# Performance work log

Hardware: AMD Instinct MI355X
Metric: run time of the kernel (lower is better)

Reference implementation:

```python
import jax, jax.numpy as jnp
import numpy as np

B, C, H, W = 4, 16, 512, 512


def setup_inputs() -> dict:
    key = jax.random.key(0)
    k1, k2, k3, k4, k5 = jax.random.split(key, 5)
    # positive depth in [0.5, 10.5] meters
    depth = jax.random.uniform(k1, (B, 1, H, W), dtype=jnp.float32) * 10.0 + 0.5
    # realistic, well-conditioned camera intrinsics per batch element
    fx = 500.0 + 20.0 * jax.random.normal(k2, (B,), dtype=jnp.float32)
    fy = 500.0 + 20.0 * jax.random.normal(k3, (B,), dtype=jnp.float32)
    zeros = jnp.zeros((B,), jnp.float32)
    ones = jnp.ones((B,), jnp.float32)
    K = jnp.stack([
        jnp.stack([fx, zeros, ones * (W / 2.0)], axis=-1),
        jnp.stack([zeros, fy, ones * (H / 2.0)], axis=-1),
        jnp.stack([zeros, zeros, ones], axis=-1),
    ], axis=1)  # [B,3,3]
    # near-identity rigid-ish transforms so homogeneous w ~ 1
    T = jnp.eye(4, dtype=jnp.float32)[None, None] + 0.05 * jax.random.normal(k4, (B, C, 4, 4), dtype=jnp.float32)
    masks = jax.random.randint(k5, (B, C, H, W), 0, 2).astype(jnp.bool_)
    return {"depth": depth, "K": K, "T": T, "masks": masks}


def reference(depth, K, T, masks):
    b, _, h, w = depth.shape
    c = masks.shape[1]
    n = h * w
    eps = 1e-10
    # --- depth -> point cloud ---
    u = jnp.arange(w, dtype=depth.dtype)
    v = jnp.arange(h, dtype=depth.dtype)
    uu, vv = jnp.meshgrid(u, v, indexing='xy')            # [H,W]
    uv1 = jnp.stack([uu, vv, jnp.ones_like(uu)], axis=-1)  # [H,W,3]
    K_inv = jnp.linalg.inv(K)                              # [B,3,3]
    d = jnp.transpose(depth, (0, 2, 3, 1))                 # [B,H,W,1]
    points_3d = jnp.einsum('bij,hwj->bhwi', K_inv, uv1) * d  # [B,H,W,3]
    # --- per-object masked transform (vectorized over all channels) ---
    pts = points_3d.reshape(b, n, 3)
    pts_h = jnp.concatenate([pts, jnp.ones((b, n, 1), pts.dtype)], axis=-1)  # [B,N,4]
    trans_h = jnp.einsum('bcij,bnj->bcni', T, pts_h)       # [B,C,N,4]
    trans3 = trans_h[..., :3] / (trans_h[..., 3:] + eps)   # [B,C,N,3]
    masks_flat = masks.reshape(b, c, n)
    out = pts
    for ci in range(c):
        out = jnp.where(masks_flat[:, ci, :, None], trans3[:, ci], out)
    tp = out.reshape(b, h, w, 3)                           # transformed points
    # --- reproject to depth map (scatter) ---
    p2h = jnp.einsum('bij,bhwj->bhwi', K, tp)              # [B,H,W,3]
    p2 = p2h[..., :2] / (p2h[..., 2:] + eps)
    Z = tp[..., 2]                                         # [B,H,W]
    u_idx = jnp.clip(p2[..., 0], 0, w - 1).astype(jnp.int32)
    v_idx = jnp.clip(p2[..., 1], 0, h - 1).astype(jnp.int32)
    b_idx = jnp.broadcast_to(jnp.arange(b)[:, None, None], (b, h, w))
    depth_map = depth.at[b_idx, 0, v_idx, u_idx].set(Z)
    return depth_map
```

## Files before the change

kernel.cpp:

```cpp
#include <hip/hip_runtime.h>
#include <stdint.h>

constexpr int B = 4, C = 16, H = 512, W = 512;
constexpr int N = H * W;
constexpr int BLOCKS_PER_BATCH = N / 256;
constexpr int NXCD = 8;
constexpr float EPS = 1e-10f;


__device__ __forceinline__ void swizzle_bn(int orig, int& b, int& blk) {
    int xcd = orig & (NXCD - 1);
    int j   = orig >> 3;
    b       = j >> 7;
    int r   = j & 127;
    blk     = xcd * 128 + r;
}

constexpr int MSTRIDE = 260;

__global__ __launch_bounds__(256) void project_atomic_kernel(
    const float* __restrict__ depth,
    const float* __restrict__ K,
    const float* __restrict__ T,
    const int*   __restrict__ masks,
    unsigned long long* __restrict__ keys)
{
    __shared__ float Ts[16][17];
    __shared__ int   Ms[16 * MSTRIDE];

    int b, blk;
    swizzle_bn(blockIdx.x, b, blk);
    int t = threadIdx.x;
    int n = (blk << 8) + t;
    int idx = b * N + n;
    int v = n >> 9;
    int u = n & (W - 1);
    int lane = t & 63;

    {
        int w = t >> 6;
        int g = t & 63;
        const int* mbase = masks + (size_t)b * C * N + (size_t)(blk << 8);
        #pragma unroll
        for (int k = 0; k < 4; ++k) {
            int c = (w << 2) + k;
            int4 m4 = *reinterpret_cast<const int4*>(mbase + (size_t)c * N + (g << 2));
            *reinterpret_cast<int4*>(&Ms[c * MSTRIDE + (g << 2)]) = m4;
        }
    }

    float d = depth[idx];

    {
        int c = t >> 4, e = t & 15;
        Ts[e][c] = T[(size_t)b * 256 + t];
    }
    __syncthreads();

    unsigned bm = 0;
    #pragma unroll
    for (int c = 0; c < 16; ++c)
        bm |= (Ms[c * MSTRIDE + t] ? 1u : 0u) << c;
    int sel = bm ? (31 - __clz(bm)) : -1;

    const float* Kb = K + b * 9;
    float k00 = Kb[0], k01 = Kb[1], k02 = Kb[2];
    float k10 = Kb[3], k11 = Kb[4], k12 = Kb[5];
    float k20 = Kb[6], k21 = Kb[7], k22 = Kb[8];

    float c00 =  (k11 * k22 - k12 * k21);
    float c01 = -(k10 * k22 - k12 * k20);
    float c02 =  (k10 * k21 - k11 * k20);
    float det = k00 * c00 + k01 * c01 + k02 * c02;
    float invdet = 1.0f / det;
    float i00 =  (k11 * k22 - k12 * k21) * invdet;
    float i01 = -(k01 * k22 - k02 * k21) * invdet;
    float i02 =  (k01 * k12 - k02 * k11) * invdet;
    float i10 = -(k10 * k22 - k12 * k20) * invdet;
    float i11 =  (k00 * k22 - k02 * k20) * invdet;
    float i12 = -(k00 * k12 - k02 * k10) * invdet;
    float i20 =  (k10 * k21 - k11 * k20) * invdet;
    float i21 = -(k00 * k21 - k01 * k20) * invdet;
    float i22 =  (k00 * k11 - k01 * k10) * invdet;

    float uf = (float)u, vf = (float)v;
    float px = (i00 * uf + i01 * vf + i02) * d;
    float py = (i10 * uf + i11 * vf + i12) * d;
    float pz = (i20 * uf + i21 * vf + i22) * d;

    float ox = px, oy = py, oz = pz;
    if (sel >= 0) {
        float tx = Ts[0][sel]*px + Ts[1][sel]*py + Ts[2][sel]*pz + Ts[3][sel];
        float ty = Ts[4][sel]*px + Ts[5][sel]*py + Ts[6][sel]*pz + Ts[7][sel];
        float tz = Ts[8][sel]*px + Ts[9][sel]*py + Ts[10][sel]*pz + Ts[11][sel];
        float tw = Ts[12][sel]*px + Ts[13][sel]*py + Ts[14][sel]*pz + Ts[15][sel];
        float denom = tw + EPS;
        ox = tx / denom;
        oy = ty / denom;
        oz = tz / denom;
    }

    float qx = k00 * ox + k01 * oy + k02 * oz;
    float qy = k10 * ox + k11 * oy + k12 * oz;
    float qz = k20 * ox + k21 * oy + k22 * oz;
    float zz = qz + EPS;
    float pu = qx / zz;
    float pv = qy / zz;
    pu = fminf(fmaxf(pu, 0.0f), (float)(W - 1));
    pv = fminf(fmaxf(pv, 0.0f), (float)(H - 1));
    int ui = (int)pu;
    int vi = (int)pv;
    unsigned tg = (unsigned)(vi * W + ui);

    bool dom = false;
    #pragma unroll
    for (int delta = 1; delta <= 4; ++delta) {
        unsigned tn = (unsigned)__shfl_down((int)tg, delta);
        dom |= (lane + delta < 64) && (tn == tg);
    }
    if (!dom) {
        unsigned long long key =
            ((unsigned long long)(unsigned)(N - 1 - n) << 32)
          | (unsigned long long)__float_as_uint(oz);
        atomicMin(&keys[(size_t)b * N + tg], key);
    }
}

__global__ __launch_bounds__(256) void resolve_kernel(
    const unsigned long long* __restrict__ keys,
    const float*              __restrict__ depth,
    float*                    __restrict__ out)
{
    int idx = blockIdx.x * blockDim.x + threadIdx.x;
    if (idx >= B * N) return;
    unsigned long long k = keys[idx];
    unsigned hi = (unsigned)(k >> 32);
    out[idx] = (hi <= (unsigned)(N - 1)) ? __uint_as_float((unsigned)k)
                                         : depth[idx];
}

extern "C" void kernel_launch(void* const* d_in, const int* in_sizes, int n_in,
                              void* d_out, int out_size, void* d_ws, size_t ws_size,
                              hipStream_t stream) {
    const float* depth = (const float*)d_in[0];
    const float* K     = (const float*)d_in[1];
    const float* T     = (const float*)d_in[2];
    const int*   masks = (const int*)d_in[3];
    float* out = (float*)d_out;

    unsigned long long* keys = (unsigned long long*)d_ws;

    int grid = B * BLOCKS_PER_BATCH;
    project_atomic_kernel<<<grid, 256, 0, stream>>>(depth, K, T, masks, keys);
    resolve_kernel<<<grid, 256, 0, stream>>>(keys, depth, out);
}
```

Baseline: 131.9 us.

## Replace global 64-bit atomics with per-slab shared-memory scatter resolve

The projection kernel now writes one packed record per pixel, holding the target index and the depth value, instead of doing a global 64-bit atomicMin. A second kernel gives each block one 32-row slab of one batch. The block scans every record of that batch, applies a 32-bit LDS atomicMin for targets inside its slab to keep the latest writer, then fills the output from the winning record or from the original depth. Mask loading also drops LDS staging in favour of direct per-thread strided loads. This removes contended global atomics and the need to initialize a key buffer. In exchange, each batch's record array is read 16 times and the resolve runs on only 64 blocks.

```diff
diff --git a/kernel.cpp b/kernel.cpp
--- a/kernel.cpp
+++ b/kernel.cpp
@@ -16,17 +16,14 @@
     blk     = xcd * 128 + r;
 }
 
-constexpr int MSTRIDE = 260;
-
-__global__ __launch_bounds__(256) void project_atomic_kernel(
+__global__ __launch_bounds__(256) void project_rec_kernel(
     const float* __restrict__ depth,
     const float* __restrict__ K,
     const float* __restrict__ T,
     const int*   __restrict__ masks,
-    unsigned long long* __restrict__ keys)
+    unsigned long long* __restrict__ recs)
 {
     __shared__ float Ts[16][17];
-    __shared__ int   Ms[16 * MSTRIDE];
 
     int b, blk;
     swizzle_bn(blockIdx.x, b, blk);
@@ -35,21 +32,12 @@
     int idx = b * N + n;
     int v = n >> 9;
     int u = n & (W - 1);
-    int lane = t & 63;
-
-    {
-        int w = t >> 6;
-        int g = t & 63;
-        const int* mbase = masks + (size_t)b * C * N + (size_t)(blk << 8);
-        #pragma unroll
-        for (int k = 0; k < 4; ++k) {
-            int c = (w << 2) + k;
-            int4 m4 = *reinterpret_cast<const int4*>(mbase + (size_t)c * N + (g << 2));
-            *reinterpret_cast<int4*>(&Ms[c * MSTRIDE + (g << 2)]) = m4;
-        }
-    }
 
     float d = depth[idx];
+    const int* mb = masks + (size_t)b * C * N + n;
+    int m[16];
+    #pragma unroll
+    for (int c = 0; c < 16; ++c) m[c] = mb[(size_t)c * N];
 
     {
         int c = t >> 4, e = t & 15;
@@ -59,8 +47,7 @@
 
     unsigned bm = 0;
     #pragma unroll
-    for (int c = 0; c < 16; ++c)
-        bm |= (Ms[c * MSTRIDE + t] ? 1u : 0u) << c;
+    for (int c = 0; c < 16; ++c) bm |= (m[c] ? 1u : 0u) << c;
     int sel = bm ? (31 - __clz(bm)) : -1;
 
     const float* Kb = K + b * 9;
@@ -112,31 +99,56 @@
     int vi = (int)pv;
     unsigned tg = (unsigned)(vi * W + ui);
 
-    bool dom = false;
-    #pragma unroll
-    for (int delta = 1; delta <= 4; ++delta) {
-        unsigned tn = (unsigned)__shfl_down((int)tg, delta);
-        dom |= (lane + delta < 64) && (tn == tg);
-    }
-    if (!dom) {
-        unsigned long long key =
-            ((unsigned long long)(unsigned)(N - 1 - n) << 32)
-          | (unsigned long long)__float_as_uint(oz);
-        atomicMin(&keys[(size_t)b * N + tg], key);
-    }
+    recs[idx] = ((unsigned long long)tg << 32)
+              | (unsigned long long)__float_as_uint(oz);
 }
 
-__global__ __launch_bounds__(256) void resolve_kernel(
-    const unsigned long long* __restrict__ keys,
+constexpr int SLAB_CELLS = 32 * W;
+constexpr int P2_THREADS = 512;
+
+__global__ __launch_bounds__(P2_THREADS) void slab_resolve_kernel(
+    const unsigned long long* __restrict__ recs,
     const float*              __restrict__ depth,
     float*                    __restrict__ out)
 {
-    int idx = blockIdx.x * blockDim.x + threadIdx.x;
-    if (idx >= B * N) return;
-    unsigned long long k = keys[idx];
-    unsigned hi = (unsigned)(k >> 32);
-    out[idx] = (hi <= (unsigned)(N - 1)) ? __uint_as_float((unsigned)k)
-                                         : depth[idx];
+    __shared__ unsigned skey[SLAB_CELLS];
+
+    int bid  = blockIdx.x;
+    int b    = bid >> 4;
+    int slab = bid & 15;
+    int tid  = threadIdx.x;
+    int lane = tid & 63;
+
+    #pragma unroll
+    for (int j = tid; j < SLAB_CELLS; j += P2_THREADS)
+        skey[j] = 0xFFFFFFFFu;
+    __syncthreads();
+
+    const unsigned long long* rb = recs + (size_t)b * N;
+
+    for (int i = tid; i < N; i += P2_THREADS) {
+        unsigned long long r = rb[i];
+        unsigned t = (unsigned)(r >> 32);
+        unsigned tn = (unsigned)__shfl_down((int)t, 1);
+        bool skip = (lane < 63) && (tn == t);
+        if (!skip && (t >> 14) == (unsigned)slab) {
+            atomicMin(&skey[t & (SLAB_CELLS - 1)], (unsigned)(N - 1 - i));
+        }
+    }
+    __syncthreads();
+
+    int out0 = b * N + slab * SLAB_CELLS;
+    for (int j = tid; j < SLAB_CELLS; j += P2_THREADS) {
+        unsigned k = skey[j];
+        float val;
+        if (k != 0xFFFFFFFFu) {
+            int n_w = N - 1 - (int)k;
+            val = __uint_as_float((unsigned)rb[n_w]);
+        } else {
+            val = depth[out0 + j];
+        }
+        out[out0 + j] = val;
+    }
 }
 
 extern "C" void kernel_launch(void* const* d_in, const int* in_sizes, int n_in,
@@ -148,9 +160,9 @@
     const int*   masks = (const int*)d_in[3];
     float* out = (float*)d_out;
 
-    unsigned long long* keys = (unsigned long long*)d_ws;
+    unsigned long long* recs = (unsigned long long*)d_ws;
 
-    int grid = B * BLOCKS_PER_BATCH;
-    project_atomic_kernel<<<grid, 256, 0, stream>>>(depth, K, T, masks, keys);
-    resolve_kernel<<<grid, 256, 0, stream>>>(keys, depth, out);
+    project_rec_kernel<<<B * BLOCKS_PER_BATCH, 256, 0, stream>>>(
+        depth, K, T, masks, recs);
+    slab_resolve_kernel<<<B * 16, P2_THREADS, 0, stream>>>(recs, depth, out);
 }
```

Result: slower. 280.9 us (+113.0%).
